# Kernel optimization log

Measured on AMD Instinct MI355X. Metric: run time of the kernel, lower is better.

The kernel has to match this reference:

```python
import jax, jax.numpy as jnp
import numpy as np

N, C, D = 64, 4, 2048
K = 64          # kernel_size (shapelet length)
O = 256         # out_channels (number of shapelets)
L = D - K + 1   # number of sliding windows


def setup_inputs() -> dict:
    key = jax.random.key(0)
    k1, k2 = jax.random.split(key)
    x_input = jax.random.normal(k1, (N, C, D), dtype=jnp.float32)
    weight = jax.random.normal(k2, (O, C, K), dtype=jnp.float32)
    return {"x_input": x_input, "weight": weight}


def reference(x_input, weight):
    # im2col: sliding windows of length K -> (n, c, L, K)
    idx = jnp.arange(L)[:, None] + jnp.arange(K)[None, :]  # (L, K)
    windows = x_input[:, :, idx]                            # (n, c, L, K)
    # pairwise squared distances per channel, normalized by K
    x_norm = jnp.sum(windows * windows, axis=-1)            # (n, c, L)
    y_norm = jnp.sum(weight * weight, axis=-1)              # (o, c)
    cross = jnp.einsum('nclk,ock->ncol', windows, weight)   # (n, c, o, L)
    dist = (x_norm[:, :, None, :] + y_norm.T[None, :, :, None] - 2.0 * cross)
    dist = jnp.maximum(dist, 0.0) / K                       # clamp(., 0, inf) / len
    return dist  # (n, in_channels, out_channels, L)
```

## Files before the change

kernel.cpp:

```cpp
#include <hip/hip_runtime.h>

#define N_ 64
#define C_ 4
#define D_ 2048
#define K_ 64
#define O_ 256
#define L_ 1985
#define XPAD 2112
#define XCOPY 2116
#define OPITCH 2020
#define NTILE 125

typedef __attribute__((ext_vector_type(8))) short s16x8;
typedef __attribute__((ext_vector_type(4))) float f32x4;

#define BAR_LGKM() do { \
    asm volatile("s_waitcnt lgkmcnt(0)\n\ts_barrier" ::: "memory"); \
    __builtin_amdgcn_sched_barrier(0); \
} while (0)

__device__ __forceinline__ unsigned short f2bf(float f) {
    union { float f; unsigned u; } v; v.f = f;
    unsigned u = v.u;
    u += 0x7fffu + ((u >> 16) & 1u);
    return (unsigned short)(u >> 16);
}

__global__ __launch_bounds__(256) void prep_w(const float* __restrict__ w,
                                              unsigned short* __restrict__ wb,
                                              float* __restrict__ yn) {
    int o = blockIdx.x;
    int tid = threadIdx.x;
    int c = tid >> 6, k = tid & 63;
    size_t idx = (size_t)(o * C_ + c) * K_ + k;
    float v = w[idx];
    wb[idx] = f2bf(v);
    float s = v * v;
    for (int off = 32; off > 0; off >>= 1) s += __shfl_down(s, off, 64);
    if (k == 0) yn[o * C_ + c] = s;
}

__global__ __launch_bounds__(1024) void shapelet_main(const float* __restrict__ x,
                                                      const unsigned short* __restrict__ wb,
                                                      const float* __restrict__ yn,
                                                      float* __restrict__ out) {
    __shared__ __align__(16) unsigned short xs[4][XCOPY];
    __shared__ float xn[D_];
    __shared__ __align__(16) float ost[16 * OPITCH];

    int nc = blockIdx.x;
    int c = nc & (C_ - 1);
    const float* xrow = x + (size_t)nc * D_;
    int tid = threadIdx.x;

    for (int i = tid; i < XPAD; i += 1024) ost[i] = (i < D_) ? xrow[i] : 0.f;
    __syncthreads();
    for (int i = tid; i < XCOPY; i += 1024) {
        #pragma unroll
        for (int s = 0; s < 4; ++s) {
            int idx = i + s;
            xs[s][i] = (idx < XPAD) ? f2bf(ost[idx]) : (unsigned short)0;
        }
    }
    for (int l = tid; l < D_; l += 1024) {
        float ssum = 0.f;
        #pragma unroll 16
        for (int k = 0; k < K_; ++k) { float v = ost[l + k]; ssum = fmaf(v, v, ssum); }
        xn[l] = ssum;
    }
    __syncthreads();

    int wave = tid >> 6, lane = tid & 63, lr = lane & 15, hi = lane >> 4;
    const unsigned short* xbase = &xs[lr & 3][(lr & ~3) + hi * 8];
    int dj = tid & 63;

    for (int st = 0; st < 16; ++st) {
        int o = st * 16 + lr;
        s16x8 wfr[2];
        #pragma unroll
        for (int kk = 0; kk < 2; ++kk)
            wfr[kk] = *reinterpret_cast<const s16x8*>(
                wb + ((size_t)o * C_ + c) * K_ + kk * 32 + hi * 8);
        float ynv = yn[o * C_ + c];

        for (int t = wave; t < NTILE; t += 16) {
            int l0t = t * 16;
            f32x4 acc = {0.f, 0.f, 0.f, 0.f};
            #pragma unroll
            for (int kk = 0; kk < 2; ++kk) {
                const unsigned long long* p =
                    (const unsigned long long*)(xbase + l0t + kk * 32);
                union { unsigned long long u[2]; s16x8 v; } a;
                a.u[0] = p[0]; a.u[1] = p[1];
                acc = __builtin_amdgcn_mfma_f32_16x16x32_bf16(a.v, wfr[kk], acc, 0, 0, 0);
            }
            f32x4 xv = *reinterpret_cast<const f32x4*>(&xn[l0t + hi * 4]);
            f32x4 r;
            #pragma unroll
            for (int j = 0; j < 4; ++j)
                r[j] = fmaxf(xv[j] + ynv - 2.f * acc[j], 0.f) * (1.f / (float)K_);
            *reinterpret_cast<f32x4*>(&ost[lr * OPITCH + l0t + hi * 4]) = r;
        }
        BAR_LGKM();

        float* gb = out + ((size_t)nc * O_ + st * 16 + wave) * L_;
        const float* src = &ost[wave * OPITCH];
        f32x4 rr[8];
        #pragma unroll
        for (int q = 0; q < 8; ++q) {
            int pos = dj * 4 + q * 256;
            if (pos + 4 <= L_) rr[q] = *reinterpret_cast<const f32x4*>(src + pos);
        }
        float tailv = (dj == 0) ? src[L_ - 1] : 0.f;
        #pragma unroll
        for (int q = 0; q < 8; ++q) {
            int pos = dj * 4 + q * 256;
            if (pos + 4 <= L_) __builtin_memcpy(gb + pos, &rr[q], 16);
        }
        if (dj == 0) gb[L_ - 1] = tailv;
        BAR_LGKM();
    }
}

extern "C" void kernel_launch(void* const* d_in, const int* in_sizes, int n_in,
                              void* d_out, int out_size, void* d_ws, size_t ws_size,
                              hipStream_t stream) {
    const float* x = (const float*)d_in[0];
    const float* w = (const float*)d_in[1];
    float* out = (float*)d_out;

    unsigned short* wb = (unsigned short*)d_ws;
    float* yn = (float*)((char*)d_ws + (size_t)O_ * C_ * K_ * 2);

    prep_w<<<O_, 256, 0, stream>>>(w, wb, yn);
    shapelet_main<<<N_ * C_, 1024, 0, stream>>>(x, wb, yn, out);
}
```

Before: 124.3 us.

## Split each row across two 512-thread blocks and align global stores to 128B

Each (n,c) row is now handled by two blocks covering halves of the window range, which doubles the grid to 512 blocks and halves shared memory per block so more blocks can be resident. The store phase is rewritten so each wave emits a scalar head up to a 32-float boundary, then aligned float4 stores, then a scalar tail, removing misaligned vector stores caused by the odd row length. Staging rows in shared memory get a per-row skew that matches this alignment. The cost is recomputing the bf16 copy and norm prologue for the overlapping halo in both blocks, plus extra scalar stores.

```diff
diff --git a/kernel.cpp b/kernel.cpp
--- a/kernel.cpp
+++ b/kernel.cpp
@@ -6,10 +6,13 @@
 #define K_ 64
 #define O_ 256
 #define L_ 1985
-#define XPAD 2112
-#define XCOPY 2116
-#define OPITCH 2020
-#define NTILE 125
+#define LB0 1024
+#define LB1 (L_ - LB0)
+#define NT0 64
+#define NT1 61
+#define XPAD2 1092
+#define XCOPY2 1096
+#define OPITCH2 1028
 
 typedef __attribute__((ext_vector_type(8))) short s16x8;
 typedef __attribute__((ext_vector_type(4))) float f32x4;
@@ -40,29 +43,37 @@
     if (k == 0) yn[o * C_ + c] = s;
 }
 
-__global__ __launch_bounds__(1024) void shapelet_main(const float* __restrict__ x,
-                                                      const unsigned short* __restrict__ wb,
-                                                      const float* __restrict__ yn,
-                                                      float* __restrict__ out) {
-    __shared__ __align__(16) unsigned short xs[4][XCOPY];
-    __shared__ float xn[D_];
-    __shared__ __align__(16) float ost[16 * OPITCH];
+__global__ __launch_bounds__(512) void shapelet_main(const float* __restrict__ x,
+                                                     const unsigned short* __restrict__ wb,
+                                                     const float* __restrict__ yn,
+                                                     float* __restrict__ out) {
+    __shared__ __align__(16) unsigned short xs[4][XCOPY2];
+    __shared__ float xn[LB0];
+    __shared__ __align__(16) float ost[16 * OPITCH2];
 
-    int nc = blockIdx.x;
+    int bid = blockIdx.x;
+    int half = bid & 1;
+    int nc = bid >> 1;
     int c = nc & (C_ - 1);
+    int l0b = half * LB0;
+    int LB = half ? LB1 : LB0;
+    int NT = half ? NT1 : NT0;
     const float* xrow = x + (size_t)nc * D_;
     int tid = threadIdx.x;
 
-    for (int i = tid; i < XPAD; i += 1024) ost[i] = (i < D_) ? xrow[i] : 0.f;
+    for (int i = tid; i < XPAD2; i += 512) {
+        int g = l0b + i;
+        ost[i] = (g < D_) ? xrow[g] : 0.f;
+    }
     __syncthreads();
-    for (int i = tid; i < XCOPY; i += 1024) {
+    for (int i = tid; i < XCOPY2; i += 512) {
         #pragma unroll
         for (int s = 0; s < 4; ++s) {
             int idx = i + s;
-            xs[s][i] = (idx < XPAD) ? f2bf(ost[idx]) : (unsigned short)0;
+            xs[s][i] = (idx < XPAD2) ? f2bf(ost[idx]) : (unsigned short)0;
         }
     }
-    for (int l = tid; l < D_; l += 1024) {
+    for (int l = tid; l < LB0; l += 512) {
         float ssum = 0.f;
         #pragma unroll 16
         for (int k = 0; k < K_; ++k) { float v = ost[l + k]; ssum = fmaf(v, v, ssum); }
@@ -72,7 +83,7 @@
 
     int wave = tid >> 6, lane = tid & 63, lr = lane & 15, hi = lane >> 4;
     const unsigned short* xbase = &xs[lr & 3][(lr & ~3) + hi * 8];
-    int dj = tid & 63;
+    int dj = lane;
 
     for (int st = 0; st < 16; ++st) {
         int o = st * 16 + lr;
@@ -83,7 +94,7 @@
                 wb + ((size_t)o * C_ + c) * K_ + kk * 32 + hi * 8);
         float ynv = yn[o * C_ + c];
 
-        for (int t = wave; t < NTILE; t += 16) {
+        for (int t = wave; t < NT; t += 8) {
             int l0t = t * 16;
             f32x4 acc = {0.f, 0.f, 0.f, 0.f};
             #pragma unroll
@@ -99,25 +110,28 @@
             #pragma unroll
             for (int j = 0; j < 4; ++j)
                 r[j] = fmaxf(xv[j] + ynv - 2.f * acc[j], 0.f) * (1.f / (float)K_);
-            *reinterpret_cast<f32x4*>(&ost[lr * OPITCH + l0t + hi * 4]) = r;
+            __builtin_memcpy(&ost[lr * OPITCH2 + (lr & 3) + l0t + hi * 4], &r, 16);
         }
         BAR_LGKM();
 
-        float* gb = out + ((size_t)nc * O_ + st * 16 + wave) * L_;
-        const float* src = &ost[wave * OPITCH];
-        f32x4 rr[8];
         #pragma unroll
-        for (int q = 0; q < 8; ++q) {
-            int pos = dj * 4 + q * 256;
-            if (pos + 4 <= L_) rr[q] = *reinterpret_cast<const f32x4*>(src + pos);
+        for (int rr2 = 0; rr2 < 2; ++rr2) {
+            int row16 = wave + rr2 * 8;
+            int r_row = st * 16 + row16;
+            float* gb = out + ((size_t)nc * O_ + r_row) * (size_t)L_ + l0b;
+            const float* src = &ost[row16 * OPITCH2 + (row16 & 3)];
+            int start = (int)(((unsigned)r_row * (unsigned)L_ + (unsigned)l0b) & 31u);
+            int h = (32 - start) & 31;
+
+            if (dj < h) gb[dj] = src[dj];
+            for (int pos = h + dj * 4; pos + 4 <= LB; pos += 256) {
+                f32x4 v = *reinterpret_cast<const f32x4*>(src + pos);
+                *reinterpret_cast<f32x4*>(gb + pos) = v;
+            }
+            int rem = (LB - h) & 3;
+            int base = LB - rem;
+            if (dj < rem) gb[base + dj] = src[base + dj];
         }
-        float tailv = (dj == 0) ? src[L_ - 1] : 0.f;
-        #pragma unroll
-        for (int q = 0; q < 8; ++q) {
-            int pos = dj * 4 + q * 256;
-            if (pos + 4 <= L_) __builtin_memcpy(gb + pos, &rr[q], 16);
-        }
-        if (dj == 0) gb[L_ - 1] = tailv;
         BAR_LGKM();
     }
 }
@@ -133,5 +147,5 @@
     float* yn = (float*)((char*)d_ws + (size_t)O_ * C_ * K_ * 2);
 
     prep_w<<<O_, 256, 0, stream>>>(w, wb, yn);
-    shapelet_main<<<N_ * C_, 1024, 0, stream>>>(x, wb, yn, out);
+    shapelet_main<<<N_ * C_ * 2, 512, 0, stream>>>(x, wb, yn, out);
 }
```

New measurement: 141.5 us. 13.8% more time.
